# Performance work log

Hardware: AMD Instinct MI355X
Metric: run time of the kernel (lower is better)

The kernel has to match this reference:

```python
import jax, jax.numpy as jnp
import numpy as np

D = 1024      # hidden_dim
V = 8         # op_vocab_size / num_ops
L = 4         # prog_len
CD = 8        # concept_dim_total (6 + 2)
I = D + CD    # op/program-generator input dim
B, T = 8, 512


def gru(x, h0, W_ih, W_hh, b_ih, b_hh):
    """PyTorch-convention GRU. x: (B,T,In), h0: (B,H). Gate order r,z,n."""
    def step(h, xt):
        gx = xt @ W_ih.T + b_ih            # (B, 3H)
        gh = h @ W_hh.T + b_hh             # (B, 3H)
        xr, xz, xn = jnp.split(gx, 3, axis=-1)
        hr, hz, hn = jnp.split(gh, 3, axis=-1)
        r = jax.nn.sigmoid(xr + hr)
        z = jax.nn.sigmoid(xz + hz)
        n = jnp.tanh(xn + r * hn)
        h_new = (1.0 - z) * n + z * h
        return h_new, h_new
    _, ys = jax.lax.scan(step, h0, jnp.swapaxes(x, 0, 1))
    return jnp.swapaxes(ys, 0, 1)          # (B,T,H)


def _l2norm(x, axis=-1):
    n = jnp.sqrt(jnp.sum(x * x, axis=axis, keepdims=True))
    return x / jnp.maximum(n, 1e-12)


def setup_inputs() -> dict:
    key = jax.random.key(0)
    ks = jax.random.split(key, 24)
    s = 0.02
    inp = {
        "x": jax.random.normal(ks[0], (B, T, D), dtype=jnp.float32),
        "attention_mask": jnp.ones((B, T), dtype=jnp.float32),
        # TemporalEncoder GRU
        "enc_Wih": s * jax.random.normal(ks[1], (3 * D, D), dtype=jnp.float32),
        "enc_Whh": s * jax.random.normal(ks[2], (3 * D, D), dtype=jnp.float32),
        "enc_bih": jnp.zeros((3 * D,), dtype=jnp.float32),
        "enc_bhh": jnp.zeros((3 * D,), dtype=jnp.float32),
        # ConceptClassifier heads (token_type=6, polarity=2)
        "tt_W": s * jax.random.normal(ks[3], (6, D), dtype=jnp.float32),
        "tt_b": jnp.zeros((6,), dtype=jnp.float32),
        "pol_W": s * jax.random.normal(ks[4], (2, D), dtype=jnp.float32),
        "pol_b": jnp.zeros((2,), dtype=jnp.float32),
        # ProgramGenerator
        "c2h_W": s * jax.random.normal(ks[5], (D, I), dtype=jnp.float32),
        "c2h_b": jnp.zeros((D,), dtype=jnp.float32),
        "pg_Wih": s * jax.random.normal(ks[6], (3 * D, I), dtype=jnp.float32),
        "pg_Whh": s * jax.random.normal(ks[7], (3 * D, D), dtype=jnp.float32),
        "pg_bih": jnp.zeros((3 * D,), dtype=jnp.float32),
        "pg_bhh": jnp.zeros((3 * D,), dtype=jnp.float32),
        "proj_W": s * jax.random.normal(ks[8], (V, D), dtype=jnp.float32),
        "proj_b": jnp.zeros((V,), dtype=jnp.float32),
        # NeuralOpLibrary: V ops, each Linear(I,D)-GELU-Linear(D,D)
        "op_W1": s * jax.random.normal(ks[9], (V, D, I), dtype=jnp.float32),
        "op_b1": jnp.zeros((V, D), dtype=jnp.float32),
        "op_W2": s * jax.random.normal(ks[10], (V, D, D), dtype=jnp.float32),
        "op_b2": jnp.zeros((V, D), dtype=jnp.float32),
        # output projection (2D -> D)
        "out_W": s * jax.random.normal(ks[11], (D, 2 * D), dtype=jnp.float32),
        "out_b": jnp.zeros((D,), dtype=jnp.float32),
    }
    return inp


def reference(x, attention_mask, enc_Wih, enc_Whh, enc_bih, enc_bhh,
              tt_W, tt_b, pol_W, pol_b, c2h_W, c2h_b,
              pg_Wih, pg_Whh, pg_bih, pg_bhh, proj_W, proj_b,
              op_W1, op_b1, op_W2, op_b2, out_W, out_b):
    Bx = x.shape[0]
    x = x * attention_mask[..., None]
    # TemporalEncoder: GRU + residual
    h0 = jnp.zeros((Bx, D), dtype=x.dtype)
    x = gru(x, h0, enc_Wih, enc_Whh, enc_bih, enc_bhh) + x        # (B,T,D)

    # concepts
    tt = x @ tt_W.T + tt_b                                        # (B,T,6)
    pol = x @ pol_W.T + pol_b                                     # (B,T,2)
    concept_summary = jnp.concatenate([tt.mean(1), pol.mean(1)], axis=-1)  # (B,8)
    pooled = x.mean(1)                                            # (B,D)
    context = jnp.concatenate([pooled, concept_summary], axis=-1) # (B,I)

    # ProgramGenerator: GRU over zero inputs, h0 from context
    pg_h0 = context @ c2h_W.T + c2h_b                             # (B,D)
    rnn_in = jnp.zeros((Bx, L, I), dtype=x.dtype)
    rnn_out = gru(rnn_in, pg_h0, pg_Wih, pg_Whh, pg_bih, pg_bhh)  # (B,L,D)
    program_logits = rnn_out @ proj_W.T + proj_b                  # (B,L,V)

    # NeuralOpLibrary. The torch code expands token feats to (B,L,T,D) and runs
    # each op redundantly per L; since op outputs are independent of L, the
    # softmax-weighted sum + mean over L equals weighting by the L-averaged
    # softmax weights (identical math).
    token_feats = jnp.concatenate([x, tt, pol], axis=-1)          # (B,T,I)
    h1 = jax.nn.gelu(jnp.einsum('bti,vdi->btvd', token_feats, op_W1) + op_b1,
                     approximate=False)                           # (B,T,V,D)
    op_out = jnp.einsum('btvh,vdh->btvd', h1, op_W2) + op_b2      # (B,T,V,D)
    w = jax.nn.softmax(program_logits, axis=-1).mean(axis=1)      # (B,V)
    out = jnp.einsum('btvd,bv->btd', op_out, w)                   # (B,T,D)

    max_pooled = out.max(axis=1)
    mean_pooled = out.mean(axis=1)
    pooled2 = jnp.concatenate([max_pooled, mean_pooled], axis=-1) # (B,2D)
    z = pooled2 @ out_W.T + out_b                                 # (B,D)

    plf = program_logits.reshape(Bx, -1)                          # (B,L*V)
    pooled_norm = _l2norm(pooled2)
    sim = pooled_norm @ pooled_norm.T                             # (B,B)
    sq = jnp.sum(plf * plf, axis=-1)
    d2 = jnp.maximum(sq[:, None] + sq[None, :] - 2.0 * (plf @ plf.T), 0.0)
    dist = jnp.where(d2 > 0, jnp.sqrt(jnp.where(d2 > 0, d2, 1.0)), 0.0)
    reuse_loss = (sim * dist).mean()

    prog_norm = _l2norm(plf)
    prog_sim = prog_norm @ prog_norm.T
    pos_mask = (sim > 0.7).astype(x.dtype)
    neg_mask = (sim < 0.7).astype(x.dtype)
    pos_loss = (1.0 - prog_sim) * pos_mask
    neg_loss = jax.nn.relu(prog_sim - 0.5) * neg_mask
    contrastive_loss = (pos_loss.sum() + neg_loss.sum()) / (pos_mask.sum() + neg_mask.sum() + 1e-6)
    return (z, reuse_loss, contrastive_loss)
```

## Files before the change

kernel.cpp:

```cpp
#include <hip/hip_runtime.h>
#include <stdint.h>

#define D_   1024
#define T_   512
#define B_   8
#define V_   8
#define I_   1032
#define KP_  1088
#define TDK  3072
#define NGRU 64
#define NHELP 192

typedef __attribute__((ext_vector_type(8))) short bf16x8;
typedef __attribute__((ext_vector_type(4))) float f32x4;

__device__ __forceinline__ ushort f2bf(float f){
  union{ unsigned u; float f; } c; c.f = f;
  unsigned u = c.u;
  return (ushort)((u + 0x7FFFu + ((u>>16)&1u)) >> 16);
}
__device__ __forceinline__ float bf2f(ushort h){
  union{ unsigned u; float f; } c; c.u = ((unsigned)h) << 16; return c.f;
}
__device__ __forceinline__ float sigmoidf_(float x){ return 1.f/(1.f+__expf(-x)); }

#define WAITV(N) do{ asm volatile("s_waitcnt vmcnt(" #N ")" ::: "memory"); __builtin_amdgcn_sched_barrier(0); }while(0)

__device__ __forceinline__ void gload_lds16(const void* g, void* l){
  __builtin_amdgcn_global_load_lds((const __attribute__((address_space(1))) void*)g,
                                   (__attribute__((address_space(3))) void*)l, 16, 0, 0);
}

__global__ __launch_bounds__(256) void k_prep(const float* __restrict__ x, const float* __restrict__ mask,
                                              float* __restrict__ xm, ushort* __restrict__ xmb){
  int i = blockIdx.x*256 + threadIdx.x;
  float4 v = ((const float4*)x)[i];
  float mk = mask[i >> 8];
  v.x*=mk; v.y*=mk; v.z*=mk; v.w*=mk;
  ((float4*)xm)[i] = v;
  ushort4 h; h.x=f2bf(v.x); h.y=f2bf(v.y); h.z=f2bf(v.z); h.w=f2bf(v.w);
  ((ushort4*)xmb)[i] = h;
}

__global__ __launch_bounds__(256) void k_hinit(unsigned* __restrict__ hw){
  hw[blockIdx.x*256 + threadIdx.x] = 1u;
}

__global__ __launch_bounds__(256) void k_cvt(const float* __restrict__ in, ushort* __restrict__ out, int n4){
  int i = blockIdx.x*256 + threadIdx.x;
  if (i < n4){
    float4 v = ((const float4*)in)[i];
    ushort4 h; h.x=f2bf(v.x); h.y=f2bf(v.y); h.z=f2bf(v.z); h.w=f2bf(v.w);
    ((ushort4*)out)[i] = h;
  }
}

struct EpiArgs {
  float* outf; ushort* outh;
  const float* bias; const float* wvp; const float* obias;
  int ldc;
};

template<int EPI, bool INIT>
__global__ __launch_bounds__(256) void k_gemm(const ushort* __restrict__ A, const ushort* __restrict__ Bm,
                                              int lda, int ldb, int K, EpiArgs e)
{
  __shared__ ushort As[128*64];
  __shared__ ushort Bs[128*64];
  const int tid = threadIdx.x;
  const int w = tid >> 6, l = tid & 63;
  const int wr = w >> 1, wc = w & 1;
  f32x4 acc[4][4] = {};
  const size_t arow = (size_t)(blockIdx.x*128);
  const size_t brow = (size_t)(blockIdx.y*128);
  const int lr = l >> 3, lcol = (l & 7) << 3;

  for (int k0 = 0; k0 < K; k0 += 64){
    __syncthreads();
    #pragma unroll
    for (int g = 0; g < 4; ++g){
      const int chunk = (g<<2) + w;
      const int row = (chunk<<3) + lr;
      gload_lds16(A + (arow + row)*lda + k0 + lcol, &As[chunk<<9]);
      gload_lds16(Bm + (brow + row)*ldb + k0 + lcol, &Bs[chunk<<9]);
    }
    __syncthreads();
    #pragma unroll
    for (int kk = 0; kk < 2; ++kk){
      bf16x8 af[4], bfr[4];
      #pragma unroll
      for (int m=0;m<4;++m) af[m]  = *(const bf16x8*)&As[(wr*64 + m*16 + (l&15))*64 + kk*32 + ((l>>4)<<3)];
      #pragma unroll
      for (int n=0;n<4;++n) bfr[n] = *(const bf16x8*)&Bs[(wc*64 + n*16 + (l&15))*64 + kk*32 + ((l>>4)<<3)];
      #pragma unroll
      for (int m=0;m<4;++m)
        #pragma unroll
        for (int n=0;n<4;++n)
          acc[m][n] = __builtin_amdgcn_mfma_f32_16x16x32_bf16(af[m], bfr[n], acc[m][n], 0, 0, 0);
    }
  }
  const int row0 = blockIdx.x*128 + wr*64 + ((l>>4)<<2);
  const int col0 = blockIdx.y*128 + wc*64 + (l&15);
  #pragma unroll
  for (int m=0;m<4;++m){
    #pragma unroll
    for (int n=0;n<4;++n){
      f32x4 a = acc[m][n];
      int col = col0 + n*16;
      #pragma unroll
      for (int q=0;q<4;++q){
        int row = row0 + m*16 + q;
        float val = a[q];
        if constexpr (EPI==1){
          float xg = val + e.bias[col];
          float g = 0.5f*xg*(1.0f + erff(xg*0.70710678118f));
          e.outh[(size_t)row*e.ldc + col] = f2bf(g * e.wvp[(row>>9)*V_ + (col>>10)]);
        } else {
          size_t idx = (size_t)row*e.ldc + col;
          float prev = INIT ? e.obias[((row>>9)<<10) + col] : e.outf[idx];
          e.outf[idx] = prev + val;
        }
      }
    }
  }
}

__global__ __launch_bounds__(256, 1) void k_mega(
    const float* __restrict__ whh, const float* __restrict__ bhh,
    const ushort* __restrict__ xmb, const ushort* __restrict__ wihb,
    const float* __restrict__ ebih, float* __restrict__ gx,
    unsigned* __restrict__ hw, const float* __restrict__ xm,
    const float* __restrict__ ttW, const float* __restrict__ ttb,
    const float* __restrict__ polW, const float* __restrict__ polb,
    ushort* __restrict__ tf, float* __restrict__ ttpol,
    const float* __restrict__ opW1, ushort* __restrict__ w1b,
    const float* __restrict__ opW2, ushort* __restrict__ w2t,
    float* __restrict__ hsum, float* __restrict__ xsum,
    int* __restrict__ done, int* __restrict__ wm)
{
  __shared__ char smem[32768];
  const int tid = threadIdx.x;
  const int w = tid >> 6, l = tid & 63;

  if (blockIdx.x < NGRU){
    const int c = blockIdx.x;
    const int ar = l & 15, kg = (l >> 4) << 3;
    ushort (*Hld)[264] = (ushort (*)[264])smem;
    float* Red = (float*)(smem + 4*8*264*2);

    bf16x8 Bf[3][8];
    #pragma unroll
    for (int g = 0; g < 3; ++g){
      #pragma unroll
      for (int s = 0; s < 8; ++s){
        const float* src = whh + ((size_t)((g<<10) + (c<<4) + ar))*1024 + (w<<8) + (s<<5) + kg;
        float4 u0 = *(const float4*)src;
        float4 u1 = *(const float4*)(src + 4);
        bf16x8 f;
        f[0]=(short)f2bf(u0.x); f[1]=(short)f2bf(u0.y); f[2]=(short)f2bf(u0.z); f[3]=(short)f2bf(u0.w);
        f[4]=(short)f2bf(u1.x); f[5]=(short)f2bf(u1.y); f[6]=(short)f2bf(u1.z); f[7]=(short)f2bf(u1.w);
        Bf[g][s] = f;
      }
    }
    const int pb = (w << 1) + ((l >> 4) & 1);
    const int pi = l & 15;
    const int dg = (c << 4) + pi;
    const float bhr = bhh[dg], bhz = bhh[1024 + dg], bhn = bhh[2048 + dg];
    float hp = 0.f, hacc = 0.f;
    __syncthreads();

    {
      const int* dp = done + l*3;
      int f0, f1, f2;
      while (true){
        asm volatile("global_load_dword %0, %1, off sc0 sc1" : "=v"(f0) : "v"(dp)   : "memory");
        asm volatile("global_load_dword %0, %1, off sc0 sc1" : "=v"(f1) : "v"(dp+1) : "memory");
        asm volatile("global_load_dword %0, %1, off sc0 sc1" : "=v"(f2) : "v"(dp+2) : "memory");
        WAITV(0);
        if (__all((f0 & f1 & f2) == 1)) break;
        __builtin_amdgcn_s_sleep(4);
      }
    }
    __syncthreads();
    float xr, xz, xn, nxr, nxz, nxn;
    if (l < 32){
      const float* g0 = gx + ((size_t)(pb*512))*TDK + dg;
      asm volatile("global_load_dword %0, %1, off sc0 sc1" : "=v"(xr) : "v"(g0)        : "memory");
      asm volatile("global_load_dword %0, %1, off sc0 sc1" : "=v"(xz) : "v"(g0 + 1024) : "memory");
      asm volatile("global_load_dword %0, %1, off sc0 sc1" : "=v"(xn) : "v"(g0 + 2048) : "memory");
    }
    WAITV(0);

    for (int t = 0; t < 512; ++t){
      if ((t & 127) == 0 && t){
        const int tq = t >> 7;
        const int* dp = done + tq*192 + l*3;
        int f0, f1, f2;
        while (true){
          asm volatile("global_load_dword %0, %1, off sc0 sc1" : "=v"(f0) : "v"(dp)   : "memory");
          asm volatile("global_load_dword %0, %1, off sc0 sc1" : "=v"(f1) : "v"(dp+1) : "memory");
          asm volatile("global_load_dword %0, %1, off sc0 sc1" : "=v"(f2) : "v"(dp+2) : "memory");
          WAITV(0);
          if (__all((f0 & f1 & f2) == 1)) break;
          __builtin_amdgcn_s_sleep(4);
        }
        __syncthreads();
        if (l < 32){
          const float* g0 = gx + ((size_t)(pb*512 + t))*TDK + dg;
          asm volatile("global_load_dword %0, %1, off sc0 sc1" : "=v"(xr) : "v"(g0)        : "memory");
          asm volatile("global_load_dword %0, %1, off sc0 sc1" : "=v"(xz) : "v"(g0 + 1024) : "memory");
          asm volatile("global_load_dword %0, %1, off sc0 sc1" : "=v"(xn) : "v"(g0 + 2048) : "memory");
        }
        WAITV(0);
      }
      uint4 rw[8];
      unsigned ok = 0;
      const unsigned tagv = (unsigned)(t + 1);
      const unsigned* qb = hw + ((size_t)t << 13) + (w << 8) + (l << 2);
      #pragma unroll
      for (int j = 0; j < 8; ++j)
        asm volatile("global_load_dwordx4 %0, %1, off sc0 sc1" : "=v"(rw[j]) : "v"(qb + (j << 10)) : "memory");
      const bool gxi = (((t+1) & 127) != 0) && (t+1 < 512);
      if (gxi && l < 32){
        const float* g0 = gx + ((size_t)(pb*512 + t + 1))*TDK + dg;
        asm volatile("global_load_dword %0, %1, off sc0 sc1" : "=v"(nxr) : "v"(g0)        : "memory");
        asm volatile("global_load_dword %0, %1, off sc0 sc1" : "=v"(nxz) : "v"(g0 + 1024) : "memory");
        asm volatile("global_load_dword %0, %1, off sc0 sc1" : "=v"(nxn) : "v"(g0 + 2048) : "memory");
      }
      if (gxi) { WAITV(3); } else { WAITV(0); }
      #pragma unroll
      for (int j = 0; j < 8; ++j){
        unsigned m = (rw[j].x ^ tagv) | (rw[j].y ^ tagv) | (rw[j].z ^ tagv) | (rw[j].w ^ tagv);
        if ((m & 0xFFFFu) == 0u) ok |= (1u << j);
      }
      while (!__all(ok == 0xFFu)){
        #pragma unroll
        for (int j = 0; j < 8; ++j){
          if (!(ok & (1u << j)))
            asm volatile("global_load_dwordx4 %0, %1, off sc0 sc1" : "=v"(rw[j]) : "v"(qb + (j << 10)) : "memory");
        }
        WAITV(0);
        #pragma unroll
        for (int j = 0; j < 8; ++j){
          if (!(ok & (1u << j))){
            unsigned m = (rw[j].x ^ tagv) | (rw[j].y ^ tagv) | (rw[j].z ^ tagv) | (rw[j].w ^ tagv);
            if ((m & 0xFFFFu) == 0u) ok |= (1u << j);
          }
        }
      }
      #pragma unroll
      for (int j = 0; j < 8; ++j){
        unsigned d0 = __builtin_amdgcn_perm(rw[j].y, rw[j].x, 0x07060302u);
        unsigned d1 = __builtin_amdgcn_perm(rw[j].w, rw[j].z, 0x07060302u);
        union { unsigned u[2]; unsigned long long ull; } cv; cv.u[0]=d0; cv.u[1]=d1;
        *(unsigned long long*)&Hld[w*8 + j][l<<2] = cv.ull;
      }
      f32x4 ac0 = {0.f,0.f,0.f,0.f}, ac1 = {0.f,0.f,0.f,0.f}, ac2 = {0.f,0.f,0.f,0.f};
      #pragma unroll
      for (int s = 0; s < 8; ++s){
        bf16x8 af = *(const bf16x8*)&Hld[w*8 + (ar & 7)][(s << 5) + kg];
        ac0 = __builtin_amdgcn_mfma_f32_16x16x32_bf16(af, Bf[0][s], ac0, 0, 0, 0);
        ac1 = __builtin_amdgcn_mfma_f32_16x16x32_bf16(af, Bf[1][s], ac1, 0, 0, 0);
        ac2 = __builtin_amdgcn_mfma_f32_16x16x32_bf16(af, Bf[2][s], ac2, 0, 0, 0);
      }
      const int cur = t & 1;
      if (l < 32){
        *(f32x4*)(&Red[cur*1536 + (w*3+0)*128 + l*4]) = ac0;
        *(f32x4*)(&Red[cur*1536 + (w*3+1)*128 + l*4]) = ac1;
        *(f32x4*)(&Red[cur*1536 + (w*3+2)*128 + l*4]) = ac2;
      }
      __syncthreads();
      if (l < 32){
        const int idx = (((pb>>2)<<4) | pi)*4 + (pb & 3);
        const float* R = Red + cur*1536;
        float ghr = R[idx]       + R[384 + idx]  + R[768 + idx]  + R[1152 + idx];
        float ghz = R[128 + idx] + R[512 + idx]  + R[896 + idx]  + R[1280 + idx];
        float ghn = R[256 + idx] + R[640 + idx]  + R[1024 + idx] + R[1408 + idx];
        float r  = sigmoidf_(xr + ghr + bhr);
        float z  = sigmoidf_(xz + ghz + bhz);
        float nn = tanhf(xn + r*(ghn + bhn));
        hp = (1.f - z)*nn + z*hp;
        hacc += hp;
        unsigned word = (((unsigned)f2bf(hp)) << 16) | (unsigned)(t + 2);
        unsigned* hdst = hw + ((size_t)(t+1) << 13) + (pb << 10) + dg;
        asm volatile("global_store_dword %0, %1, off sc0 sc1" :: "v"(hdst), "v"(word) : "memory");
      }
      if (c == 0 && tid == 0){
        asm volatile("global_store_dword %0, %1, off sc0 sc1" :: "v"(wm), "v"(t) : "memory");
      }
      if (gxi && l < 32){ xr = nxr; xz = nxz; xn = nxn; }
    }
    if (l < 32) hsum[(pb << 10) + dg] = hacc;
    return;
  }

  const int hid = blockIdx.x - NGRU;
  ushort* As = (ushort*)smem;
  ushort* Bs = As + 8192;

  {
    const int bb = hid / 24, ni = hid % 24;
    const int wr_ = w >> 1, wc_ = w & 1;
    const int lr = l >> 3, lcol = (l & 7) << 3;
    for (int wv = 0; wv < 4; ++wv){
      const int mi = bb*4 + wv;
      f32x4 acc[4][4] = {};
      for (int k0 = 0; k0 < 1024; k0 += 64){
        __syncthreads();
        #pragma unroll
        for (int g = 0; g < 4; ++g){
          const int chunk = (g<<2) + w;
          const int row = (chunk<<3) + lr;
          gload_lds16(xmb + (size_t)(mi*128 + row)*1024 + k0 + lcol, &As[chunk<<9]);
          gload_lds16(wihb + (size_t)(ni*128 + row)*1024 + k0 + lcol, &Bs[chunk<<9]);
        }
        __syncthreads();
        #pragma unroll
        for (int kk = 0; kk < 2; ++kk){
          bf16x8 af[4], bfr[4];
          #pragma unroll
          for (int m=0;m<4;++m) af[m]  = *(const bf16x8*)&As[(wr_*64 + m*16 + (l&15))*64 + kk*32 + ((l>>4)<<3)];
          #pragma unroll
          for (int n=0;n<4;++n) bfr[n] = *(const bf16x8*)&Bs[(wc_*64 + n*16 + (l&15))*64 + kk*32 + ((l>>4)<<3)];
          #pragma unroll
          for (int m=0;m<4;++m)
            #pragma unroll
            for (int n=0;n<4;++n)
              acc[m][n] = __builtin_amdgcn_mfma_f32_16x16x32_bf16(af[m], bfr[n], acc[m][n], 0, 0, 0);
        }
      }
      const int row0 = mi*128 + wr_*64 + ((l>>4)<<2);
      const int col0 = ni*128 + wc_*64 + (l&15);
      #pragma unroll
      for (int m=0;m<4;++m){
        #pragma unroll
        for (int n=0;n<4;++n){
          f32x4 a = acc[m][n];
          int col = col0 + n*16;
          float bi = ebih[col];
          #pragma unroll
          for (int q=0;q<4;++q){
            int row = row0 + m*16 + q;
            float val = a[q] + bi;
            float* p = gx + (size_t)row*TDK + col;
            asm volatile("global_store_dword %0, %1, off sc0 sc1" :: "v"(p), "v"(val) : "memory");
          }
        }
      }
      WAITV(0);
      __syncthreads();
      if (tid == 0){
        int one = 1;
        const int* fp = done + wv*192 + hid;
        asm volatile("global_store_dword %0, %1, off sc0 sc1" :: "v"(fp), "v"(one) : "memory");
      }
      __syncthreads();
    }
  }
  for (int row = hid; row < 8192; row += NHELP){
    const float* src = opW1 + (size_t)row*I_;
    ushort* dst = w1b + (size_t)row*KP_;
    for (int cc = tid; cc < KP_; cc += 256){
      float v = (cc < I_) ? src[cc] : 0.f;
      dst[cc] = f2bf(v);
    }
  }
  for (int blk = hid; blk < 8192; blk += NHELP){
    const int v = blk >> 10, d = blk & 1023;
    const float4* src = (const float4*)(opW2 + ((size_t)(v*1024 + d))*1024);
    ushort* dst = w2t + (size_t)d*8192 + v*1024;
    float4 u = src[tid];
    ushort4 h; h.x=f2bf(u.x); h.y=f2bf(u.y); h.z=f2bf(u.z); h.w=f2bf(u.w);
    ((ushort4*)dst)[tid] = h;
  }
  if (hid < 32){
    const int o = hid*256 + tid;
    const int b = o >> 10, d = o & 1023;
    float s = 0.f;
    for (int t = 0; t < 512; ++t) s += xm[((size_t)(b*512 + t) << 10) + d];
    xsum[o] = s;
  }
  {
    float* xe = (float*)smem;
    for (int idx = hid; idx < 4096; idx += NHELP){
      const int t = idx >> 3, b = idx & 7;
      const int tok = b*512 + t;
      const int need = (t+1 < 511) ? (t+1) : 511;
      if (tid == 0){
        int wmv;
        while (true){
          asm volatile("global_load_dword %0, %1, off sc0 sc1" : "=v"(wmv) : "v"(wm) : "memory");
          asm volatile("s_waitcnt vmcnt(0)" ::: "memory");
          if (wmv >= need) break;
          __builtin_amdgcn_s_sleep(64);
        }
      }
      __syncthreads();
      const unsigned tagv = (unsigned)(t + 2);
      const unsigned* src = hw + ((size_t)(t+1) << 13) + (b << 10) + (tid << 2);
      uint4 hv;
      while (true){
        asm volatile("global_load_dwordx4 %0, %1, off sc0 sc1" : "=v"(hv) : "v"(src) : "memory");
        WAITV(0);
        unsigned m = (hv.x ^ tagv) | (hv.y ^ tagv) | (hv.z ^ tagv) | (hv.w ^ tagv);
        if (__syncthreads_and((int)((m & 0xFFFFu) == 0u))) break;
        __builtin_amdgcn_s_sleep(16);
      }
      float4 xv = ((const float4*)(xm + (size_t)tok*1024))[tid];
      float4 ev;
      ev.x = bf2f((ushort)(hv.x >> 16)) + xv.x;
      ev.y = bf2f((ushort)(hv.y >> 16)) + xv.y;
      ev.z = bf2f((ushort)(hv.z >> 16)) + xv.z;
      ev.w = bf2f((ushort)(hv.w >> 16)) + xv.w;
      *(float4*)&xe[tid*4] = ev;
      ushort4 eb; eb.x=f2bf(ev.x); eb.y=f2bf(ev.y); eb.z=f2bf(ev.z); eb.w=f2bf(ev.w);
      *(ushort4*)&tf[(size_t)tok*KP_ + tid*4] = eb;
      __syncthreads();
      const int j = tid >> 5, ln = tid & 31;
      const float* Wr = (j < 6) ? (ttW + j*1024) : (polW + (j-6)*1024);
      float acc = 0.f;
      for (int k = ln; k < 1024; k += 32) acc += xe[k]*Wr[k];
      #pragma unroll
      for (int m=16; m>=1; m>>=1) acc += __shfl_xor(acc, m, 32);
      if (ln == 0){
        float val = acc + ((j<6)? ttb[j] : polb[j-6]);
        ttpol[(size_t)tok*8 + j] = val;
        tf[(size_t)tok*KP_ + 1024 + j] = f2bf(val);
      }
      if (tid < 56) tf[(size_t)tok*KP_ + 1032 + tid] = 0;
      __syncthreads();
    }
  }
}

__global__ __launch_bounds__(64) void k_csum(const float* __restrict__ ttpol, float* __restrict__ csum){
  const int b = threadIdx.x >> 3, j = threadIdx.x & 7;
  float s = 0.f;
  for (int t=0; t<512; ++t) s += ttpol[((size_t)(b*512+t)<<3) + j];
  csum[threadIdx.x] = s * (1.f/512.f);
}

__global__ __launch_bounds__(256) void k_ctx(const float* __restrict__ hsum, const float* __restrict__ xsum,
                                             const float* __restrict__ csum,
                                             const float* __restrict__ c2hW, const float* __restrict__ c2hb,
                                             float* __restrict__ pgh0){
  const int i = blockIdx.x*256 + threadIdx.x;
  const int b = i >> 10, d = i & 1023;
  const float* wr = c2hW + (size_t)d*I_;
  const float* hs = hsum + (b<<10);
  const float* xs = xsum + (b<<10);
  float s = 0.f;
  for (int k=0; k<1024; ++k) s += (hs[k]+xs[k])*wr[k];
  float acc = c2hb[d] + s*(1.f/512.f);
  #pragma unroll
  for (int k=0; k<8; ++k) acc += csum[b*8+k]*wr[1024+k];
  pgh0[i] = acc;
}

__global__ __launch_bounds__(256) void k_pg(const float* __restrict__ whh, const float* __restrict__ bih,
                                            const float* __restrict__ bhh, const float* __restrict__ hin,
                                            float* __restrict__ hout){
  __shared__ float sh[8][1024];
  const int tid = threadIdx.x;
  for (int f = tid; f < 2048; f += 256) ((float4*)&sh[0][0])[f] = ((const float4*)hin)[f];
  __syncthreads();
  const int d = blockIdx.x*8 + (tid>>5), ln = tid & 31;
  const float* wr = whh + (size_t)d*1024;
  const float* wz = whh + (size_t)(1024+d)*1024;
  const float* wn = whh + (size_t)(2048+d)*1024;
  float ar[8]={0,0,0,0,0,0,0,0}, az[8]={0,0,0,0,0,0,0,0}, an[8]={0,0,0,0,0,0,0,0};
  for (int k = ln; k < 1024; k += 32){
    float r_=wr[k], z_=wz[k], n_=wn[k];
    #pragma unroll
    for (int b=0;b<8;++b){ float h = sh[b][k]; ar[b]+=h*r_; az[b]+=h*z_; an[b]+=h*n_; }
  }
  #pragma unroll
  for (int m=16; m>=1; m>>=1){
    #pragma unroll
    for (int b=0;b<8;++b){ ar[b]+=__shfl_xor(ar[b],m,32); az[b]+=__shfl_xor(az[b],m,32); an[b]+=__shfl_xor(an[b],m,32); }
  }
  if (ln == 0){
    float xr=bih[d], xz=bih[1024+d], xn=bih[2048+d];
    float br=bhh[d], bz=bhh[1024+d], bn=bhh[2048+d];
    #pragma unroll
    for (int b=0;b<8;++b){
      float r = sigmoidf_(xr + ar[b] + br);
      float z = sigmoidf_(xz + az[b] + bz);
      float nn = tanhf(xn + r*(an[b] + bn));
      hout[(b<<10)+d] = (1.f - z)*nn + z*sh[b][d];
    }
  }
}

__global__ __launch_bounds__(256) void k_wlogits(const float* __restrict__ pgh, const float* __restrict__ prjW,
                                                 const float* __restrict__ prjb, float* __restrict__ plog,
                                                 float* __restrict__ wv){
  __shared__ float lg[256];
  __shared__ float sm[256];
  const int tid = threadIdx.x;
  const int b = tid>>5, li = (tid>>3)&3, v = tid&7;
  const float* h = pgh + (size_t)(li+1)*8192 + (b<<10);
  const float* pw = prjW + (v<<10);
  float acc = prjb[v];
  for (int k=0;k<1024;++k) acc += h[k]*pw[k];
  lg[tid] = acc;
  plog[tid] = acc;
  __syncthreads();
  if (tid < 32){
    const int bb = tid>>2, ll = tid&3;
    const float* row = &lg[bb*32 + ll*8];
    float mx = row[0];
    #pragma unroll
    for (int u=1;u<8;++u) mx = fmaxf(mx, row[u]);
    float e[8], s=0.f;
    #pragma unroll
    for (int u=0;u<8;++u){ e[u]=__expf(row[u]-mx); s+=e[u]; }
    #pragma unroll
    for (int u=0;u<8;++u) sm[(bb*4+ll)*8+u] = e[u]/s;
  }
  __syncthreads();
  if (tid < 64){
    const int bb = tid>>3, u = tid&7;
    float s = sm[(bb*4+0)*8+u] + sm[(bb*4+1)*8+u] + sm[(bb*4+2)*8+u] + sm[(bb*4+3)*8+u];
    wv[bb*8+u] = 0.25f*s;
  }
}

__global__ __launch_bounds__(256) void k_obias(const float* __restrict__ wv, const float* __restrict__ opb2,
                                               float* __restrict__ obias){
  const int i = blockIdx.x*256 + threadIdx.x;
  const int b = i>>10, d = i&1023;
  float s = 0.f;
  #pragma unroll
  for (int v=0; v<8; ++v) s += wv[b*8+v]*opb2[(v<<10)+d];
  obias[i] = s;
}

__global__ __launch_bounds__(128) void k_pool2(const float* __restrict__ outb, float* __restrict__ pooled2){
  const int b = blockIdx.x >> 3;
  const int col = ((blockIdx.x & 7) << 7) + threadIdx.x;
  float mx = -3.4e38f, sm = 0.f;
  for (int t=0; t<512; ++t){
    float v = outb[((size_t)(b*512+t)<<10) + col];
    mx = fmaxf(mx, v); sm += v;
  }
  pooled2[((size_t)b<<11) + col] = mx;
  pooled2[((size_t)b<<11) + 1024 + col] = sm*(1.f/512.f);
}

__global__ __launch_bounds__(256) void k_z(const float* __restrict__ pooled2, const float* __restrict__ outW,
                                           const float* __restrict__ outBias, float* __restrict__ dout){
  __shared__ float p2[2048];
  const int o = blockIdx.x << 3;
  const int b = o >> 10, dbase = o & 1023;
  for (int f = threadIdx.x; f < 512; f += 256)
    ((float4*)p2)[f] = ((const float4*)(pooled2 + ((size_t)b<<11)))[f];
  __syncthreads();
  const int g = threadIdx.x >> 5, ln = threadIdx.x & 31;
  const int d = dbase + g;
  const float* wr = outW + ((size_t)d << 11);
  float acc = 0.f;
  for (int k = ln; k < 2048; k += 32) acc += p2[k]*wr[k];
  #pragma unroll
  for (int m=16; m>=1; m>>=1) acc += __shfl_xor(acc, m, 32);
  if (ln == 0) dout[(b<<10) + d] = acc + outBias[d];
}

__global__ __launch_bounds__(64) void k_losses(const float* __restrict__ p2g, const float* __restrict__ plog,
                                               float* __restrict__ dout){
  __shared__ float p2n[8], sq[8], pn[8];
  const int l = threadIdx.x;
  { const int b=l>>3, p=l&7; float s=0.f;
    const float* row = p2g + ((size_t)b<<11) + (p<<8);
    for (int k=0;k<256;++k){ float v=row[k]; s += v*v; }
    s += __shfl_xor(s,4,8); s += __shfl_xor(s,2,8); s += __shfl_xor(s,1,8);
    if (p==0) p2n[b] = fmaxf(sqrtf(s), 1e-12f);
  }
  if (l < 8){
    float s=0.f;
    #pragma unroll
    for (int k=0;k<32;++k){ float v=plog[l*32+k]; s+=v*v; }
    sq[l]=s; pn[l]=fmaxf(sqrtf(s),1e-12f);
  }
  __syncthreads();
  const int i=l>>3, j=l&7;
  const float* ri = p2g + ((size_t)i<<11);
  const float* rj = p2g + ((size_t)j<<11);
  float dot=0.f; for (int k=0;k<2048;++k) dot += ri[k]*rj[k];
  float sim = dot/(p2n[i]*p2n[j]);
  float pd=0.f;
  #pragma unroll
  for (int k=0;k<32;++k) pd += plog[i*32+k]*plog[j*32+k];
  float d2 = fmaxf(sq[i]+sq[j]-2.f*pd, 0.f);
  float dist = (d2>0.f)? sqrtf(d2) : 0.f;
  float psim = pd/(pn[i]*pn[j]);
  float pos = (sim>0.7f)?1.f:0.f, neg = (sim<0.7f)?1.f:0.f;
  float rs = sim*dist, ps=(1.f-psim)*pos, ns=fmaxf(psim-0.5f,0.f)*neg, pc=pos, nc=neg;
  #pragma unroll
  for (int m=32; m>=1; m>>=1){
    rs+=__shfl_xor(rs,m); ps+=__shfl_xor(ps,m); ns+=__shfl_xor(ns,m);
    pc+=__shfl_xor(pc,m); nc+=__shfl_xor(nc,m);
  }
  if (l==0){ dout[8192]=rs*(1.f/64.f); dout[8193]=(ps+ns)/(pc+nc+1e-6f); }
}

extern "C" void kernel_launch(void* const* d_in, const int* in_sizes, int n_in,
                              void* d_out, int out_size, void* d_ws, size_t ws_size,
                              hipStream_t stream) {
  (void)in_sizes; (void)n_in; (void)out_size; (void)ws_size;
  const float* x     = (const float*)d_in[0];
  const float* amask = (const float*)d_in[1];
  const float* eWih  = (const float*)d_in[2];
  const float* eWhh  = (const float*)d_in[3];
  const float* ebih  = (const float*)d_in[4];
  const float* ebhh  = (const float*)d_in[5];
  const float* ttW   = (const float*)d_in[6];
  const float* ttb   = (const float*)d_in[7];
  const float* polW  = (const float*)d_in[8];
  const float* polb  = (const float*)d_in[9];
  const float* c2hW  = (const float*)d_in[10];
  const float* c2hb  = (const float*)d_in[11];
  const float* pgWhh = (const float*)d_in[13];
  const float* pgbih = (const float*)d_in[14];
  const float* pgbhh = (const float*)d_in[15];
  const float* prjW  = (const float*)d_in[16];
  const float* prjb  = (const float*)d_in[17];
  const float* opW1  = (const float*)d_in[18];
  const float* opb1  = (const float*)d_in[19];
  const float* opW2  = (const float*)d_in[20];
  const float* opb2  = (const float*)d_in[21];
  const float* outW  = (const float*)d_in[22];
  const float* outB  = (const float*)d_in[23];
  float* dout = (float*)d_out;

  char* ws = (char*)d_ws;
  size_t off = 0;
  auto alloc = [&](size_t bytes)->void*{ void* p = ws + off; off += (bytes + 255) & ~(size_t)255; return p; };
  char*     R       = (char*)   alloc(64ULL*1024*1024);
  float*    xm      = (float*)  R;
  float*    gx      = (float*) (R + 16ULL*1024*1024);
  ushort*   h1g     = (ushort*) R;
  ushort*   xmb     = (ushort*)  alloc(4096ULL*1024*2);
  ushort*   wihb    = (ushort*)  alloc(3072ULL*1024*2);
  unsigned* hw      = (unsigned*)alloc(513ULL*8192*4);
  float*    ttpol   = (float*)   alloc(4096ULL*8*4);
  ushort*   tf      = (ushort*)  alloc(4096ULL*KP_*2);
  ushort*   w1b     = (ushort*)  alloc(8ULL*1024*KP_*2);
  ushort*   w2t     = (ushort*)  alloc(1024ULL*8192*2);
  float*    outbuf  = (float*)   alloc(4096ULL*1024*4);
  float*    hsum    = (float*)   alloc(8192*4);
  float*    xsum    = (float*)   alloc(8192*4);
  float*    csum    = (float*)   alloc(64*4);
  float*    pgh     = (float*)   alloc(5ULL*8192*4);
  float*    plog    = (float*)   alloc(256*4);
  float*    wv      = (float*)   alloc(64*4);
  float*    obias   = (float*)   alloc(8192*4);
  float*    pooled2 = (float*)   alloc(16384*4);
  int*      ctrl    = (int*)     alloc(4096);
  int*      done    = ctrl;
  int*      wm      = ctrl + 896;

  hipMemsetAsync(done, 0, 4*192*4, stream);
  hipMemsetAsync(wm, 0xFF, 4, stream);
  k_hinit<<<32, 256, 0, stream>>>(hw);
  k_prep<<<4096, 256, 0, stream>>>(x, amask, xm, xmb);
  k_cvt<<<3072, 256, 0, stream>>>(eWih, wihb, 3072*1024/4);

  k_mega<<<256, 256, 0, stream>>>(eWhh, ebhh, xmb, wihb, ebih, gx, hw, xm,
                                  ttW, ttb, polW, polb, tf, ttpol,
                                  opW1, w1b, opW2, w2t, hsum, xsum, done, wm);

  k_csum<<<1, 64, 0, stream>>>(ttpol, csum);
  k_ctx<<<32, 256, 0, stream>>>(hsum, xsum, csum, c2hW, c2hb, pgh);
  for (int t = 0; t < 4; ++t)
    k_pg<<<128, 256, 0, stream>>>(pgWhh, pgbih, pgbhh, pgh + (size_t)t*8192, pgh + (size_t)(t+1)*8192);
  k_wlogits<<<1, 256, 0, stream>>>(pgh, prjW, prjb, plog, wv);
  k_obias<<<32, 256, 0, stream>>>(wv, opb2, obias);

  { EpiArgs e{}; e.outh = h1g; e.bias = opb1; e.wvp = wv; e.ldc = 8192;
    k_gemm<1,false><<<dim3(32,64), 256, 0, stream>>>(tf, w1b, KP_, KP_, KP_, e); }
  { EpiArgs e{}; e.outf = outbuf; e.obias = obias; e.ldc = 1024;
    k_gemm<2,true><<<dim3(32,8), 256, 0, stream>>>(h1g, w2t, 8192, 8192, 8192, e); }

  k_pool2<<<64, 128, 0, stream>>>(outbuf, pooled2);
  k_z<<<1024, 256, 0, stream>>>(pooled2, outW, outB, dout);
  k_losses<<<1, 64, 0, stream>>>(pooled2, plog, dout);
}
```

Baseline: 1.624 ms.

## Halve GRU recurrence blocks, each block owning 32 hidden units

The persistent GRU recurrence moves from 64 blocks of 16 hidden columns to 32 blocks of 32 columns. Each block now keeps twice the recurrent-weight fragments in registers, runs six MFMA chains per k-step, and all 256 threads take part in the gate math. The aim is to halve the number of blocks that poll for and exchange the hidden state each timestep, which cuts global synchronisation traffic on the serial critical path. The cost is more register pressure, more LDS for the reduction buffer, and twice the per-block MFMA work each step. The extra helper blocks are guarded so they idle in the GEMM phase.

```diff
diff --git a/kernel.cpp b/kernel.cpp
--- a/kernel.cpp
+++ b/kernel.cpp
@@ -8,8 +8,8 @@
 #define I_   1032
 #define KP_  1088
 #define TDK  3072
-#define NGRU 64
-#define NHELP 192
+#define NGRU 32
+#define NHELP 224
 
 typedef __attribute__((ext_vector_type(8))) short bf16x8;
 typedef __attribute__((ext_vector_type(4))) float f32x4;
@@ -138,35 +138,39 @@
     float* __restrict__ hsum, float* __restrict__ xsum,
     int* __restrict__ done, int* __restrict__ wm)
 {
-  __shared__ char smem[32768];
+  __shared__ char smem[41600];
   const int tid = threadIdx.x;
   const int w = tid >> 6, l = tid & 63;
 
   if (blockIdx.x < NGRU){
-    const int c = blockIdx.x;
+    const int slot = blockIdx.x;
+    ushort (*Hld)[264] = (ushort (*)[264])smem;
+    float* Red = (float*)(smem + 16896);
     const int ar = l & 15, kg = (l >> 4) << 3;
-    ushort (*Hld)[264] = (ushort (*)[264])smem;
-    float* Red = (float*)(smem + 4*8*264*2);
-
-    bf16x8 Bf[3][8];
-    #pragma unroll
-    for (int g = 0; g < 3; ++g){
-      #pragma unroll
-      for (int s = 0; s < 8; ++s){
-        const float* src = whh + ((size_t)((g<<10) + (c<<4) + ar))*1024 + (w<<8) + (s<<5) + kg;
+
+    bf16x8 Bf[6][8];
+    #pragma unroll
+    for (int f = 0; f < 6; ++f){
+      const int rr = f*16 + (l & 15);
+      const int g = rr >> 5, i = rr & 31;
+      #pragma unroll
+      for (int ks = 0; ks < 8; ++ks){
+        const float* src = whh + ((size_t)((g<<10) + (slot<<5) + i))*1024 + (w<<8) + (ks<<5) + kg;
         float4 u0 = *(const float4*)src;
         float4 u1 = *(const float4*)(src + 4);
-        bf16x8 f;
-        f[0]=(short)f2bf(u0.x); f[1]=(short)f2bf(u0.y); f[2]=(short)f2bf(u0.z); f[3]=(short)f2bf(u0.w);
-        f[4]=(short)f2bf(u1.x); f[5]=(short)f2bf(u1.y); f[6]=(short)f2bf(u1.z); f[7]=(short)f2bf(u1.w);
-        Bf[g][s] = f;
-      }
-    }
-    const int pb = (w << 1) + ((l >> 4) & 1);
-    const int pi = l & 15;
-    const int dg = (c << 4) + pi;
+        bf16x8 fr;
+        fr[0]=(short)f2bf(u0.x); fr[1]=(short)f2bf(u0.y); fr[2]=(short)f2bf(u0.z); fr[3]=(short)f2bf(u0.w);
+        fr[4]=(short)f2bf(u1.x); fr[5]=(short)f2bf(u1.y); fr[6]=(short)f2bf(u1.z); fr[7]=(short)f2bf(u1.w);
+        Bf[f][ks] = fr;
+      }
+    }
+    const int gb = tid >> 5, gi = tid & 31;
+    const int dg = (slot << 5) + gi;
+    const int n_ = gi & 15, fb = gi >> 4;
+    const int idxc = (((gb>>2)<<4) + n_)*4 + (gb & 3);
     const float bhr = bhh[dg], bhz = bhh[1024 + dg], bhn = bhh[2048 + dg];
     float hp = 0.f, hacc = 0.f;
+    float xr, xz, xn, nxr, nxz, nxn;
     __syncthreads();
 
     {
@@ -182,9 +186,8 @@
       }
     }
     __syncthreads();
-    float xr, xz, xn, nxr, nxz, nxn;
-    if (l < 32){
-      const float* g0 = gx + ((size_t)(pb*512))*TDK + dg;
+    {
+      const float* g0 = gx + ((size_t)(gb*512))*TDK + dg;
       asm volatile("global_load_dword %0, %1, off sc0 sc1" : "=v"(xr) : "v"(g0)        : "memory");
       asm volatile("global_load_dword %0, %1, off sc0 sc1" : "=v"(xz) : "v"(g0 + 1024) : "memory");
       asm volatile("global_load_dword %0, %1, off sc0 sc1" : "=v"(xn) : "v"(g0 + 2048) : "memory");
@@ -205,8 +208,8 @@
           __builtin_amdgcn_s_sleep(4);
         }
         __syncthreads();
-        if (l < 32){
-          const float* g0 = gx + ((size_t)(pb*512 + t))*TDK + dg;
+        {
+          const float* g0 = gx + ((size_t)(gb*512 + t))*TDK + dg;
           asm volatile("global_load_dword %0, %1, off sc0 sc1" : "=v"(xr) : "v"(g0)        : "memory");
           asm volatile("global_load_dword %0, %1, off sc0 sc1" : "=v"(xz) : "v"(g0 + 1024) : "memory");
           asm volatile("global_load_dword %0, %1, off sc0 sc1" : "=v"(xn) : "v"(g0 + 2048) : "memory");
@@ -221,8 +224,8 @@
       for (int j = 0; j < 8; ++j)
         asm volatile("global_load_dwordx4 %0, %1, off sc0 sc1" : "=v"(rw[j]) : "v"(qb + (j << 10)) : "memory");
       const bool gxi = (((t+1) & 127) != 0) && (t+1 < 512);
-      if (gxi && l < 32){
-        const float* g0 = gx + ((size_t)(pb*512 + t + 1))*TDK + dg;
+      if (gxi){
+        const float* g0 = gx + ((size_t)(gb*512 + t + 1))*TDK + dg;
         asm volatile("global_load_dword %0, %1, off sc0 sc1" : "=v"(nxr) : "v"(g0)        : "memory");
         asm volatile("global_load_dword %0, %1, off sc0 sc1" : "=v"(nxz) : "v"(g0 + 1024) : "memory");
         asm volatile("global_load_dword %0, %1, off sc0 sc1" : "=v"(nxn) : "v"(g0 + 2048) : "memory");
@@ -255,42 +258,46 @@
         union { unsigned u[2]; unsigned long long ull; } cv; cv.u[0]=d0; cv.u[1]=d1;
         *(unsigned long long*)&Hld[w*8 + j][l<<2] = cv.ull;
       }
-      f32x4 ac0 = {0.f,0.f,0.f,0.f}, ac1 = {0.f,0.f,0.f,0.f}, ac2 = {0.f,0.f,0.f,0.f};
-      #pragma unroll
-      for (int s = 0; s < 8; ++s){
-        bf16x8 af = *(const bf16x8*)&Hld[w*8 + (ar & 7)][(s << 5) + kg];
-        ac0 = __builtin_amdgcn_mfma_f32_16x16x32_bf16(af, Bf[0][s], ac0, 0, 0, 0);
-        ac1 = __builtin_amdgcn_mfma_f32_16x16x32_bf16(af, Bf[1][s], ac1, 0, 0, 0);
-        ac2 = __builtin_amdgcn_mfma_f32_16x16x32_bf16(af, Bf[2][s], ac2, 0, 0, 0);
+      f32x4 ac[6] = {};
+      #pragma unroll
+      for (int ks = 0; ks < 8; ++ks){
+        bf16x8 af = *(const bf16x8*)&Hld[w*8 + (ar & 7)][(ks << 5) + kg];
+        #pragma unroll
+        for (int f = 0; f < 6; ++f)
+          ac[f] = __builtin_amdgcn_mfma_f32_16x16x32_bf16(af, Bf[f][ks], ac[f], 0, 0, 0);
       }
       const int cur = t & 1;
       if (l < 32){
-        *(f32x4*)(&Red[cur*1536 + (w*3+0)*128 + l*4]) = ac0;
-        *(f32x4*)(&Red[cur*1536 + (w*3+1)*128 + l*4]) = ac1;
-        *(f32x4*)(&Red[cur*1536 + (w*3+2)*128 + l*4]) = ac2;
+        float* Rb = Red + cur*3072 + w*768;
+        #pragma unroll
+        for (int f = 0; f < 6; ++f) *(f32x4*)(Rb + f*128 + l*4) = ac[f];
       }
       __syncthreads();
-      if (l < 32){
-        const int idx = (((pb>>2)<<4) | pi)*4 + (pb & 3);
-        const float* R = Red + cur*1536;
-        float ghr = R[idx]       + R[384 + idx]  + R[768 + idx]  + R[1152 + idx];
-        float ghz = R[128 + idx] + R[512 + idx]  + R[896 + idx]  + R[1280 + idx];
-        float ghn = R[256 + idx] + R[640 + idx]  + R[1024 + idx] + R[1408 + idx];
+      {
+        const float* R = Red + cur*3072;
+        float ghr = 0.f, ghz = 0.f, ghn = 0.f;
+        #pragma unroll
+        for (int ww = 0; ww < 4; ++ww){
+          const float* Rw = R + ww*768;
+          ghr += Rw[(0*2 + fb)*128 + idxc];
+          ghz += Rw[(1*2 + fb)*128 + idxc];
+          ghn += Rw[(2*2 + fb)*128 + idxc];
+        }
         float r  = sigmoidf_(xr + ghr + bhr);
         float z  = sigmoidf_(xz + ghz + bhz);
         float nn = tanhf(xn + r*(ghn + bhn));
         hp = (1.f - z)*nn + z*hp;
         hacc += hp;
         unsigned word = (((unsigned)f2bf(hp)) << 16) | (unsigned)(t + 2);
-        unsigned* hdst = hw + ((size_t)(t+1) << 13) + (pb << 10) + dg;
+        unsigned* hdst = hw + ((size_t)(t+1) << 13) + (gb << 10) + dg;
         asm volatile("global_store_dword %0, %1, off sc0 sc1" :: "v"(hdst), "v"(word) : "memory");
       }
-      if (c == 0 && tid == 0){
+      if (slot == 0 && tid == 0){
         asm volatile("global_store_dword %0, %1, off sc0 sc1" :: "v"(wm), "v"(t) : "memory");
       }
-      if (gxi && l < 32){ xr = nxr; xz = nxz; xn = nxn; }
-    }
-    if (l < 32) hsum[(pb << 10) + dg] = hacc;
+      if (gxi){ xr = nxr; xz = nxz; xn = nxn; }
+    }
+    hsum[(gb << 10) + dg] = hacc;
     return;
   }
 
@@ -298,7 +305,7 @@
   ushort* As = (ushort*)smem;
   ushort* Bs = As + 8192;
 
-  {
+  if (hid < 192){
     const int bb = hid / 24, ni = hid % 24;
     const int wr_ = w >> 1, wc_ = w & 1;
     const int lr = l >> 3, lcol = (l & 7) << 3;
```

New measurement: 1.759 ms. 1.08x slower.

## Stream first op-MLP GEMM into helper blocks overlapping the GRU recurrence

Applied to the files above, without the earlier changes.

Helper blocks in the persistent mega-kernel now compute the first op-MLP GEMM (tf x W1 plus GELU) tile by tile while the GRU scan is still running. Each tile waits on per-token and per-W1-row completion flags, and results go to a separate h1 buffer. The per-(b,v) scaling by wv, which needs data only available later, moves into a new elementwise k_scale pass. This hides most of the large GEMM behind the latency-bound recurrence, at the cost of an extra read/write pass over h1, unpipelined GEMM tiles that load through registers, and a dependence on workspace size that selects the path.

```diff
diff --git a/kernel.cpp b/kernel.cpp
--- a/kernel.cpp
+++ b/kernel.cpp
@@ -30,6 +30,10 @@
   __builtin_amdgcn_global_load_lds((const __attribute__((address_space(1))) void*)g,
                                    (__attribute__((address_space(3))) void*)l, 16, 0, 0);
 }
+__device__ __forceinline__ void st_dwordx2_sc(void* p, unsigned lo, unsigned hi){
+  uint2 v; v.x = lo; v.y = hi;
+  asm volatile("global_store_dwordx2 %0, %1, off sc0 sc1" :: "v"(p), "v"(v) : "memory");
+}
 
 __global__ __launch_bounds__(256) void k_prep(const float* __restrict__ x, const float* __restrict__ mask,
                                               float* __restrict__ xm, ushort* __restrict__ xmb){
@@ -53,6 +57,17 @@
     ushort4 h; h.x=f2bf(v.x); h.y=f2bf(v.y); h.z=f2bf(v.z); h.w=f2bf(v.w);
     ((ushort4*)out)[i] = h;
   }
+}
+
+__global__ __launch_bounds__(256) void k_scale(ushort* __restrict__ h1g, const float* __restrict__ wv){
+  const int i = blockIdx.x*256 + threadIdx.x;
+  const int b = i >> 20;
+  const int v = (i >> 8) & 7;
+  const float s = wv[b*8 + v];
+  ushort4 h = ((const ushort4*)h1g)[i];
+  h.x = f2bf(bf2f(h.x)*s); h.y = f2bf(bf2f(h.y)*s);
+  h.z = f2bf(bf2f(h.z)*s); h.w = f2bf(bf2f(h.w)*s);
+  ((ushort4*)h1g)[i] = h;
 }
 
 struct EpiArgs {
@@ -135,8 +150,10 @@
     ushort* __restrict__ tf, float* __restrict__ ttpol,
     const float* __restrict__ opW1, ushort* __restrict__ w1b,
     const float* __restrict__ opW2, ushort* __restrict__ w2t,
+    const float* __restrict__ opb1, ushort* __restrict__ h1g,
     float* __restrict__ hsum, float* __restrict__ xsum,
-    int* __restrict__ done, int* __restrict__ wm)
+    int* __restrict__ done, int* __restrict__ wm,
+    int* __restrict__ tfdone, int* __restrict__ w1done, int stream)
 {
   __shared__ char smem[32768];
   const int tid = threadIdx.x;
@@ -357,21 +374,38 @@
       __syncthreads();
     }
   }
-  for (int row = hid; row < 8192; row += NHELP){
-    const float* src = opW1 + (size_t)row*I_;
-    ushort* dst = w1b + (size_t)row*KP_;
-    for (int cc = tid; cc < KP_; cc += 256){
-      float v = (cc < I_) ? src[cc] : 0.f;
-      dst[cc] = f2bf(v);
-    }
-  }
-  for (int blk = hid; blk < 8192; blk += NHELP){
-    const int v = blk >> 10, d = blk & 1023;
-    const float4* src = (const float4*)(opW2 + ((size_t)(v*1024 + d))*1024);
-    ushort* dst = w2t + (size_t)d*8192 + v*1024;
-    float4 u = src[tid];
-    ushort4 h; h.x=f2bf(u.x); h.y=f2bf(u.y); h.z=f2bf(u.z); h.w=f2bf(u.w);
-    ((ushort4*)dst)[tid] = h;
+  if (hid >= 160){
+    for (int row = hid - 160; row < 8192; row += 32){
+      const float* src = opW1 + (size_t)row*I_;
+      ushort* dst = w1b + (size_t)row*KP_;
+      for (int c0 = tid*4; c0 < KP_; c0 += 1024){
+        ushort4 h;
+        h.x = (c0   < I_) ? f2bf(src[c0])   : (ushort)0;
+        h.y = (c0+1 < I_) ? f2bf(src[c0+1]) : (ushort)0;
+        h.z = (c0+2 < I_) ? f2bf(src[c0+2]) : (ushort)0;
+        h.w = (c0+3 < I_) ? f2bf(src[c0+3]) : (ushort)0;
+        unsigned lo = ((unsigned)h.y << 16) | h.x;
+        unsigned hi = ((unsigned)h.w << 16) | h.z;
+        st_dwordx2_sc(dst + c0, lo, hi);
+      }
+    }
+    WAITV(0);
+    __syncthreads();
+    if (tid == 0){
+      int one = 1;
+      const int* fp = w1done + (hid - 160);
+      asm volatile("global_store_dword %0, %1, off sc0 sc1" :: "v"(fp), "v"(one) : "memory");
+    }
+  }
+  if (hid >= 128 && hid < 160){
+    for (int blk = hid - 128; blk < 8192; blk += 32){
+      const int v = blk >> 10, d = blk & 1023;
+      const float4* src = (const float4*)(opW2 + ((size_t)(v*1024 + d))*1024);
+      ushort* dst = w2t + (size_t)d*8192 + v*1024;
+      float4 u = src[tid];
+      ushort4 h; h.x=f2bf(u.x); h.y=f2bf(u.y); h.z=f2bf(u.z); h.w=f2bf(u.w);
+      ((ushort4*)dst)[tid] = h;
+    }
   }
   if (hid < 32){
     const int o = hid*256 + tid;
@@ -380,55 +414,148 @@
     for (int t = 0; t < 512; ++t) s += xm[((size_t)(b*512 + t) << 10) + d];
     xsum[o] = s;
   }
-  {
-    float* xe = (float*)smem;
-    for (int idx = hid; idx < 4096; idx += NHELP){
-      const int t = idx >> 3, b = idx & 7;
-      const int tok = b*512 + t;
-      const int need = (t+1 < 511) ? (t+1) : 511;
-      if (tid == 0){
-        int wmv;
+  for (int tb = 0; tb < 4; ++tb){
+    {
+      float* xe = (float*)smem;
+      for (int idx = tb*1024 + hid; idx < (tb+1)*1024; idx += NHELP){
+        const int t = idx >> 3, b = idx & 7;
+        const int tok = b*512 + t;
+        const int need = (t+1 < 511) ? (t+1) : 511;
+        if (tid == 0){
+          int wmv;
+          while (true){
+            asm volatile("global_load_dword %0, %1, off sc0 sc1" : "=v"(wmv) : "v"(wm) : "memory");
+            asm volatile("s_waitcnt vmcnt(0)" ::: "memory");
+            if (wmv >= need) break;
+            __builtin_amdgcn_s_sleep(64);
+          }
+        }
+        __syncthreads();
+        const unsigned tagv = (unsigned)(t + 2);
+        const unsigned* src = hw + ((size_t)(t+1) << 13) + (b << 10) + (tid << 2);
+        uint4 hv;
         while (true){
-          asm volatile("global_load_dword %0, %1, off sc0 sc1" : "=v"(wmv) : "v"(wm) : "memory");
-          asm volatile("s_waitcnt vmcnt(0)" ::: "memory");
-          if (wmv >= need) break;
-          __builtin_amdgcn_s_sleep(64);
-        }
-      }
-      __syncthreads();
-      const unsigned tagv = (unsigned)(t + 2);
-      const unsigned* src = hw + ((size_t)(t+1) << 13) + (b << 10) + (tid << 2);
-      uint4 hv;
-      while (true){
-        asm volatile("global_load_dwordx4 %0, %1, off sc0 sc1" : "=v"(hv) : "v"(src) : "memory");
+          asm volatile("global_load_dwordx4 %0, %1, off sc0 sc1" : "=v"(hv) : "v"(src) : "memory");
+          WAITV(0);
+          unsigned m = (hv.x ^ tagv) | (hv.y ^ tagv) | (hv.z ^ tagv) | (hv.w ^ tagv);
+          if (__syncthreads_and((int)((m & 0xFFFFu) == 0u))) break;
+          __builtin_amdgcn_s_sleep(16);
+        }
+        float4 xv = ((const float4*)(xm + (size_t)tok*1024))[tid];
+        float4 ev;
+        ev.x = bf2f((ushort)(hv.x >> 16)) + xv.x;
+        ev.y = bf2f((ushort)(hv.y >> 16)) + xv.y;
+        ev.z = bf2f((ushort)(hv.z >> 16)) + xv.z;
+        ev.w = bf2f((ushort)(hv.w >> 16)) + xv.w;
+        *(float4*)&xe[tid*4] = ev;
+        ushort4 eb; eb.x=f2bf(ev.x); eb.y=f2bf(ev.y); eb.z=f2bf(ev.z); eb.w=f2bf(ev.w);
+        {
+          unsigned lo = ((unsigned)eb.y << 16) | eb.x;
+          unsigned hi = ((unsigned)eb.w << 16) | eb.z;
+          st_dwordx2_sc(&tf[(size_t)tok*KP_ + tid*4], lo, hi);
+        }
+        __syncthreads();
+        const int j = tid >> 5, ln = tid & 31;
+        const float* Wr = (j < 6) ? (ttW + j*1024) : (polW + (j-6)*1024);
+        float acc = 0.f;
+        for (int k = ln; k < 1024; k += 32) acc += xe[k]*Wr[k];
+        #pragma unroll
+        for (int m=16; m>=1; m>>=1) acc += __shfl_xor(acc, m, 32);
+        if (ln == 0){
+          float val = acc + ((j<6)? ttb[j] : polb[j-6]);
+          ttpol[(size_t)tok*8 + j] = val;
+          ushort hv2 = f2bf(val);
+          asm volatile("global_store_short %0, %1, off sc0 sc1" :: "v"(&tf[(size_t)tok*KP_ + 1024 + j]), "v"((unsigned)hv2) : "memory");
+        }
+        if (tid < 56){
+          asm volatile("global_store_short %0, %1, off sc0 sc1" :: "v"(&tf[(size_t)tok*KP_ + 1032 + tid]), "v"(0u) : "memory");
+        }
         WAITV(0);
-        unsigned m = (hv.x ^ tagv) | (hv.y ^ tagv) | (hv.z ^ tagv) | (hv.w ^ tagv);
-        if (__syncthreads_and((int)((m & 0xFFFFu) == 0u))) break;
-        __builtin_amdgcn_s_sleep(16);
-      }
-      float4 xv = ((const float4*)(xm + (size_t)tok*1024))[tid];
-      float4 ev;
-      ev.x = bf2f((ushort)(hv.x >> 16)) + xv.x;
-      ev.y = bf2f((ushort)(hv.y >> 16)) + xv.y;
-      ev.z = bf2f((ushort)(hv.z >> 16)) + xv.z;
-      ev.w = bf2f((ushort)(hv.w >> 16)) + xv.w;
-      *(float4*)&xe[tid*4] = ev;
-      ushort4 eb; eb.x=f2bf(ev.x); eb.y=f2bf(ev.y); eb.z=f2bf(ev.z); eb.w=f2bf(ev.w);
-      *(ushort4*)&tf[(size_t)tok*KP_ + tid*4] = eb;
-      __syncthreads();
-      const int j = tid >> 5, ln = tid & 31;
-      const float* Wr = (j < 6) ? (ttW + j*1024) : (polW + (j-6)*1024);
-      float acc = 0.f;
-      for (int k = ln; k < 1024; k += 32) acc += xe[k]*Wr[k];
-      #pragma unroll
-      for (int m=16; m>=1; m>>=1) acc += __shfl_xor(acc, m, 32);
-      if (ln == 0){
-        float val = acc + ((j<6)? ttb[j] : polb[j-6]);
-        ttpol[(size_t)tok*8 + j] = val;
-        tf[(size_t)tok*KP_ + 1024 + j] = f2bf(val);
-      }
-      if (tid < 56) tf[(size_t)tok*KP_ + 1032 + tid] = 0;
-      __syncthreads();
+        __syncthreads();
+        if (tid == 0){
+          int one = 1;
+          asm volatile("global_store_dword %0, %1, off sc0 sc1" :: "v"(tfdone + idx), "v"(one) : "memory");
+        }
+        __syncthreads();
+      }
+    }
+    if (stream){
+      const int wr_ = w >> 1, wc_ = w & 1;
+      const int lr = l >> 3, lcol = (l & 7) << 3;
+      for (int u2 = hid; u2 < 512; u2 += NHELP){
+        const int b = u2 >> 6, n = u2 & 63;
+        {
+          while (true){
+            int f0 = 1;
+            if (tid < 32){
+              asm volatile("global_load_dword %0, %1, off sc0 sc1" : "=v"(f0) : "v"(w1done + tid) : "memory");
+              asm volatile("s_waitcnt vmcnt(0)" ::: "memory");
+            } else if (tid < 160){
+              const int idx = (tb*128 + (tid - 32))*8 + b;
+              asm volatile("global_load_dword %0, %1, off sc0 sc1" : "=v"(f0) : "v"(tfdone + idx) : "memory");
+              asm volatile("s_waitcnt vmcnt(0)" ::: "memory");
+            }
+            if (__syncthreads_and((int)(f0 == 1))) break;
+            __builtin_amdgcn_s_sleep(16);
+          }
+        }
+        const size_t arow = (size_t)(b*512 + tb*128);
+        const size_t brow = (size_t)(n*128);
+        f32x4 acc[4][4] = {};
+        for (int k0 = 0; k0 < KP_; k0 += 64){
+          __syncthreads();
+          uint4 va[4], vb[4];
+          #pragma unroll
+          for (int g = 0; g < 4; ++g){
+            const int chunk = (g<<2) + w;
+            const int row = (chunk<<3) + lr;
+            const ushort* pa = tf  + (arow + row)*KP_ + k0 + lcol;
+            const ushort* pb = w1b + (brow + row)*KP_ + k0 + lcol;
+            asm volatile("global_load_dwordx4 %0, %1, off sc0 sc1" : "=v"(va[g]) : "v"(pa) : "memory");
+            asm volatile("global_load_dwordx4 %0, %1, off sc0 sc1" : "=v"(vb[g]) : "v"(pb) : "memory");
+          }
+          WAITV(0);
+          #pragma unroll
+          for (int g = 0; g < 4; ++g){
+            const int chunk = (g<<2) + w;
+            *(uint4*)&As[(chunk<<9) + l*8] = va[g];
+            *(uint4*)&Bs[(chunk<<9) + l*8] = vb[g];
+          }
+          __syncthreads();
+          #pragma unroll
+          for (int kk = 0; kk < 2; ++kk){
+            bf16x8 af[4], bfr[4];
+            #pragma unroll
+            for (int m=0;m<4;++m) af[m]  = *(const bf16x8*)&As[(wr_*64 + m*16 + (l&15))*64 + kk*32 + ((l>>4)<<3)];
+            #pragma unroll
+            for (int nn=0;nn<4;++nn) bfr[nn] = *(const bf16x8*)&Bs[(wc_*64 + nn*16 + (l&15))*64 + kk*32 + ((l>>4)<<3)];
+            #pragma unroll
+            for (int m=0;m<4;++m)
+              #pragma unroll
+              for (int nn=0;nn<4;++nn)
+                acc[m][nn] = __builtin_amdgcn_mfma_f32_16x16x32_bf16(af[m], bfr[nn], acc[m][nn], 0, 0, 0);
+          }
+        }
+        const int row0 = (int)arow + wr_*64 + ((l>>4)<<2);
+        const int col0 = (int)brow + wc_*64 + (l&15);
+        #pragma unroll
+        for (int m=0;m<4;++m){
+          #pragma unroll
+          for (int nn=0;nn<4;++nn){
+            f32x4 a = acc[m][nn];
+            int col = col0 + nn*16;
+            float bi = opb1[col];
+            #pragma unroll
+            for (int q=0;q<4;++q){
+              int row = row0 + m*16 + q;
+              float xg = a[q] + bi;
+              float g = 0.5f*xg*(1.0f + erff(xg*0.70710678118f));
+              h1g[(size_t)row*8192 + col] = f2bf(g);
+            }
+          }
+        }
+        __syncthreads();
+      }
     }
   }
 }
@@ -607,7 +734,7 @@
 extern "C" void kernel_launch(void* const* d_in, const int* in_sizes, int n_in,
                               void* d_out, int out_size, void* d_ws, size_t ws_size,
                               hipStream_t stream) {
-  (void)in_sizes; (void)n_in; (void)out_size; (void)ws_size;
+  (void)in_sizes; (void)n_in; (void)out_size;
   const float* x     = (const float*)d_in[0];
   const float* amask = (const float*)d_in[1];
   const float* eWih  = (const float*)d_in[2];
@@ -639,7 +766,6 @@
   char*     R       = (char*)   alloc(64ULL*1024*1024);
   float*    xm      = (float*)  R;
   float*    gx      = (float*) (R + 16ULL*1024*1024);
-  ushort*   h1g     = (ushort*) R;
   ushort*   xmb     = (ushort*)  alloc(4096ULL*1024*2);
   ushort*   wihb    = (ushort*)  alloc(3072ULL*1024*2);
   unsigned* hw      = (unsigned*)alloc(513ULL*8192*4);
@@ -656,11 +782,15 @@
   float*    wv      = (float*)   alloc(64*4);
   float*    obias   = (float*)   alloc(8192*4);
   float*    pooled2 = (float*)   alloc(16384*4);
-  int*      ctrl    = (int*)     alloc(4096);
+  int*      ctrl    = (int*)     alloc(32768);
   int*      done    = ctrl;
   int*      wm      = ctrl + 896;
-
-  hipMemsetAsync(done, 0, 4*192*4, stream);
+  int*      tfdone  = ctrl + 1024;
+  int*      w1done  = ctrl + 5120;
+  const int do_stream = (ws_size >= off + 64ULL*1024*1024 + (1<<20)) ? 1 : 0;
+  ushort*   h1g     = do_stream ? (ushort*)alloc(4096ULL*8192*2) : (ushort*)R;
+
+  hipMemsetAsync(ctrl, 0, 5152*4, stream);
   hipMemsetAsync(wm, 0xFF, 4, stream);
   k_hinit<<<32, 256, 0, stream>>>(hw);
   k_prep<<<4096, 256, 0, stream>>>(x, amask, xm, xmb);
@@ -668,7 +798,8 @@
 
   k_mega<<<256, 256, 0, stream>>>(eWhh, ebhh, xmb, wihb, ebih, gx, hw, xm,
                                   ttW, ttb, polW, polb, tf, ttpol,
-                                  opW1, w1b, opW2, w2t, hsum, xsum, done, wm);
+                                  opW1, w1b, opW2, w2t, opb1, h1g,
+                                  hsum, xsum, done, wm, tfdone, w1done, do_stream);
 
   k_csum<<<1, 64, 0, stream>>>(ttpol, csum);
   k_ctx<<<32, 256, 0, stream>>>(hsum, xsum, csum, c2hW, c2hb, pgh);
@@ -677,10 +808,14 @@
   k_wlogits<<<1, 256, 0, stream>>>(pgh, prjW, prjb, plog, wv);
   k_obias<<<32, 256, 0, stream>>>(wv, opb2, obias);
 
-  { EpiArgs e{}; e.outh = h1g; e.bias = opb1; e.wvp = wv; e.ldc = 8192;
-    k_gemm<1,false><<<dim3(32,64), 256, 0, stream>>>(tf, w1b, KP_, KP_, KP_, e); }
-  { EpiArgs e{}; e.outf = outbuf; e.obias = obias; e.ldc = 1024;
-    k_gemm<2,true><<<dim3(32,8), 256, 0, stream>>>(h1g, w2t, 8192, 8192, 8192, e); }
+  if (do_stream){
+    k_scale<<<32768, 256, 0, stream>>>(h1g, wv);
+  } else {
+    EpiArgs e1{}; e1.outh = h1g; e1.bias = opb1; e1.wvp = wv; e1.ldc = 8192;
+    k_gemm<1,false><<<dim3(32,64), 256, 0, stream>>>(tf, w1b, KP_, KP_, KP_, e1);
+  }
+  { EpiArgs e2{}; e2.outf = outbuf; e2.obias = obias; e2.ldc = 1024;
+    k_gemm<2,true><<<dim3(32,8), 256, 0, stream>>>(h1g, w2t, 8192, 8192, 8192, e2); }
 
   k_pool2<<<64, 128, 0, stream>>>(outbuf, pooled2);
   k_z<<<1024, 256, 0, stream>>>(pooled2, outW, outB, dout);
```

Measured after the change: 1.630 ms. Within noise of the previous version (+0.4%).
